# Performance work log

Hardware: AMD Instinct MI355X
Metric: run time of the kernel (lower is better)

The kernel has to match this reference:

```python
import jax, jax.numpy as jnp
import numpy as np

N_NODES = 100000
N_EDGES = 1000000
IN_DIM, HID_DIM, OUT_DIM = 256, 128, 128


def setup_inputs() -> dict:
    key = jax.random.key(0)
    ks = jax.random.split(key, 6)
    return {
        "x1": jax.random.normal(ks[0], (N_NODES, IN_DIM), jnp.float32),
        "edge_index1": jax.random.randint(ks[1], (2, N_EDGES), 0, N_NODES, jnp.int64),
        "x2": jax.random.normal(ks[2], (N_NODES, IN_DIM), jnp.float32),
        "edge_index2": jax.random.randint(ks[3], (2, N_EDGES), 0, N_NODES, jnp.int64),
        "W0": jax.random.normal(ks[4], (IN_DIM, HID_DIM), jnp.float32) * (1.0 / np.sqrt(IN_DIM)),
        "b0": jnp.zeros((HID_DIM,), jnp.float32),
        "W1": jax.random.normal(ks[5], (HID_DIM, OUT_DIM), jnp.float32) * (1.0 / np.sqrt(HID_DIM)),
        "b1": jnp.zeros((OUT_DIM,), jnp.float32),
        "p1": 0,
        "p2": 0,
    }


def _gcn_backbone(x, edge_index, W0, b0, W1, b1):
    # PyG GCNConv: add self-loops, symmetric norm D^-1/2 (A+I) D^-1/2,
    # h = x @ W, aggregate src->dst, add bias.
    n = x.shape[0]
    loops = jnp.arange(n, dtype=edge_index.dtype)
    src = jnp.concatenate([edge_index[0], loops])
    dst = jnp.concatenate([edge_index[1], loops])
    deg = jax.ops.segment_sum(jnp.ones_like(dst, jnp.float32), dst, num_segments=n)
    dinv = jnp.where(deg > 0, jax.lax.rsqrt(deg), 0.0)
    coef = (dinv[src] * dinv[dst])[:, None]  # [E+n, 1]

    def conv(h, W, b):
        h = h @ W  # [n, d_out]
        return jax.ops.segment_sum(h[src] * coef, dst, num_segments=n) + b

    h = jax.nn.relu(conv(x, W0, b0))
    # dropout with p=0 / eval mode is identity
    return conv(h, W1, b1)


def _colnorm(h):
    # (h - mean(0)) / std(0), torch std is unbiased (ddof=1)
    mu = h.mean(axis=0)
    sd = h.std(axis=0, ddof=1)
    return (h - mu) / sd


def reference(x1, edge_index1, x2, edge_index2, W0, b0, W1, b1, p1, p2):
    h1 = _gcn_backbone(x1, edge_index1, W0, b0, W1, b1)
    h2 = _gcn_backbone(x2, edge_index2, W0, b0, W1, b1)
    return _colnorm(h1), _colnorm(h2)
```

## Files before the change

### kernel.cpp

```cpp
#include <hip/hip_runtime.h>

#define CDIV(a,b) (((a)+(b)-1)/(b))

typedef __bf16 bf16x8 __attribute__((ext_vector_type(8)));
typedef float  f32x4  __attribute__((ext_vector_type(4)));

__device__ __forceinline__ ushort f2bf(float f) {
    uint u = __float_as_uint(f);
    uint r = u + 0x7fffu + ((u >> 16) & 1u);
    return (ushort)(r >> 16);
}
__device__ __forceinline__ float bf_lo(uint p) { return __uint_as_float(p << 16); }
__device__ __forceinline__ float bf_hi(uint p) { return __uint_as_float(p & 0xffff0000u); }


__global__ __launch_bounds__(256) void binA_k(const int* __restrict__ src,
                                              const int* __restrict__ dst, int E,
                                              int NB, int CAP,
                                              int* __restrict__ bcur,
                                              uint* __restrict__ binned) {
    __shared__ uint hist[512];
    __shared__ uint cur[512];
    const int t = threadIdx.x;
    for (int i = t; i < NB; i += 256) hist[i] = 0;
    __syncthreads();

    const int e0 = blockIdx.x * 4096;
    const int e1 = min(e0 + 4096, E);
    for (int e = e0 + t; e < e1; e += 256)
        atomicAdd(&hist[dst[e] >> 8], 1u);
    __syncthreads();

    for (int i = t; i < NB; i += 256) {
        uint c = hist[i];
        cur[i] = c ? (uint)atomicAdd(&bcur[i], (int)c) : 0u;
    }
    __syncthreads();

    for (int e = e0 + t; e < e1; e += 256) {
        int d = dst[e];
        int b = d >> 8;
        uint p = atomicAdd(&cur[b], 1u);
        if (p < (uint)CAP)
            binned[(size_t)b * CAP + p] = ((uint)src[e] << 8) | (uint)(d & 255);
    }
}

__global__ __launch_bounds__(256) void binB_k(const uint* __restrict__ binned,
                                              const int* __restrict__ bcur,
                                              int N, int CAP,
                                              int* __restrict__ csr,
                                              int* __restrict__ start,
                                              int* __restrict__ degc,
                                              float* __restrict__ dinv) {
    __shared__ uint hist[256];
    __shared__ uint cur[256];
    __shared__ uint wsum[4];
    const int b = blockIdx.x;
    const int t = threadIdx.x;
    int cnt = bcur[b];
    if (cnt > CAP) cnt = CAP;
    const uint* be = binned + (size_t)b * CAP;

    hist[t] = 0;
    __syncthreads();
    for (int e = t; e < cnt; e += 256) atomicAdd(&hist[be[e] & 255u], 1u);
    __syncthreads();

    uint v = hist[t];
    uint inc = v;
#pragma unroll
    for (int off = 1; off < 64; off <<= 1) {
        uint n = __shfl_up(inc, off);
        if ((t & 63) >= off) inc += n;
    }
    if ((t & 63) == 63) wsum[t >> 6] = inc;
    __syncthreads();
    uint wo = 0;
    if ((t >> 6) >= 1) wo += wsum[0];
    if ((t >> 6) >= 2) wo += wsum[1];
    if ((t >> 6) >= 3) wo += wsum[2];
    uint excl = wo + inc - v;
    cur[t] = excl;
    __syncthreads();

    const int base = b * CAP;
    for (int e = t; e < cnt; e += 256) {
        uint w = be[e];
        uint p = atomicAdd(&cur[w & 255u], 1u);
        csr[base + (int)p] = (int)(w >> 8);
    }

    int node = b * 256 + t;
    if (node < N) {
        start[node] = base + (int)excl;
        degc[node]  = (int)v;
        dinv[node]  = rsqrtf((float)(v + 1));
    }
}


__global__ __launch_bounds__(256) void pack_w_k(const float* __restrict__ W,
                                                ushort* __restrict__ Wp, int K) {
    int idx = blockIdx.x * 256 + threadIdx.x;
    int total = (K / 32) * 8 * 64;
    if (idx >= total) return;
    int l  = idx & 63;
    int nf = (idx >> 6) & 7;
    int kb = idx >> 9;
    int col = nf * 16 + (l & 15);
    int k0  = kb * 32 + (l >> 4) * 8;
    ushort o[8];
#pragma unroll
    for (int j = 0; j < 8; ++j) o[j] = f2bf(W[(size_t)(k0 + j) * 128 + col]);
    *reinterpret_cast<float4*>(Wp + (size_t)idx * 8) = *reinterpret_cast<float4*>(o);
}


template <int K, typename TIn>
__global__ __launch_bounds__(256) void gemm_mfma(const TIn* __restrict__ X,
                                                 const float4* __restrict__ Wp,
                                                 const float* __restrict__ dinv,
                                                 ushort* __restrict__ C, int N) {
    constexpr int SLOTS = K / 8;
    __shared__ ushort As[128 * K];

    const int t    = threadIdx.x;
    const int lane = t & 63;
    const int w    = t >> 6;
    const int row0 = blockIdx.x * 128;

    for (int i = t; i < 128 * SLOTS; i += 256) {
        int r = i / SLOTS;
        int c = i % SLOTS;
        int grow = row0 + r;
        ushort av[8];
        if (grow < N) {
            if constexpr (sizeof(TIn) == 4) {
                const float* px = (const float*)X + (size_t)grow * K + c * 8;
                float4 v0 = *reinterpret_cast<const float4*>(px);
                float4 v1 = *reinterpret_cast<const float4*>(px + 4);
                av[0] = f2bf(v0.x); av[1] = f2bf(v0.y); av[2] = f2bf(v0.z); av[3] = f2bf(v0.w);
                av[4] = f2bf(v1.x); av[5] = f2bf(v1.y); av[6] = f2bf(v1.z); av[7] = f2bf(v1.w);
            } else {
                const ushort* px = (const ushort*)X + (size_t)grow * K + c * 8;
                *reinterpret_cast<float4*>(av) = *reinterpret_cast<const float4*>(px);
            }
        } else {
#pragma unroll
            for (int j = 0; j < 8; ++j) av[j] = 0;
        }
        int cs = c ^ (r & 7);
        *reinterpret_cast<float4*>(&As[r * K + cs * 8]) = *reinterpret_cast<float4*>(av);
    }
    __syncthreads();

    f32x4 acc[2][8] = {};

#pragma unroll
    for (int kb = 0; kb < K / 32; ++kb) {
        bf16x8 bfr[8];
#pragma unroll
        for (int nf = 0; nf < 8; ++nf)
            bfr[nf] = *reinterpret_cast<const bf16x8*>(Wp + (size_t)(kb * 8 + nf) * 64 + lane);
#pragma unroll
        for (int mf = 0; mf < 2; ++mf) {
            int r = w * 32 + mf * 16 + (lane & 15);
            int c = kb * 4 + (lane >> 4);
            int cs = c ^ (r & 7);
            bf16x8 a = *reinterpret_cast<const bf16x8*>(&As[r * K + cs * 8]);
#pragma unroll
            for (int nf = 0; nf < 8; ++nf)
                acc[mf][nf] = __builtin_amdgcn_mfma_f32_16x16x32_bf16(a, bfr[nf], acc[mf][nf], 0, 0, 0);
        }
    }

#pragma unroll
    for (int mf = 0; mf < 2; ++mf) {
        const int rb = row0 + w * 32 + mf * 16 + ((lane >> 4) << 2);
#pragma unroll
        for (int i = 0; i < 4; ++i) {
            int row = rb + i;
            if (row < N) {
                float dr = dinv[row];
#pragma unroll
                for (int nf = 0; nf < 8; ++nf)
                    C[(size_t)row * 128 + nf * 16 + (lane & 15)] = f2bf(acc[mf][nf][i] * dr);
            }
        }
    }
}


template <int RELU, typename TOut>
__global__ __launch_bounds__(256) void agg_k(const ushort* __restrict__ Hin,
                                             TOut* __restrict__ Hout,
                                             const int* __restrict__ csr,
                                             const int* __restrict__ start,
                                             const int* __restrict__ degc,
                                             const float* __restrict__ dinv,
                                             const float* __restrict__ bias,
                                             int N) {
    const int wid  = threadIdx.x >> 6;
    const int lane = threadIdx.x & 63;
    const int v = blockIdx.x * 4 + wid;
    if (v >= N) return;

    float dv = dinv[v];
    int s   = start[v];
    int end = s + degc[v];

    const uint* base = reinterpret_cast<const uint*>(Hin);
    uint hp = base[(size_t)v * 64 + lane];
    float ax = bf_lo(hp);
    float ay = bf_hi(hp);

    for (int bs = s; bs < end; bs += 64) {
        int m = end - bs;
        if (m > 64) m = 64;
        int u_l = 0;
        if (lane < m) u_l = csr[bs + lane];
        int e = 0;
        for (; e + 8 <= m; e += 8) {
            uint p[8];
#pragma unroll
            for (int j = 0; j < 8; ++j) {
                int u = __shfl(u_l, e + j);
                p[j] = base[(size_t)u * 64 + lane];
            }
#pragma unroll
            for (int j = 0; j < 8; ++j) { ax += bf_lo(p[j]); ay += bf_hi(p[j]); }
        }
        if (e + 4 <= m) {
            uint p[4];
#pragma unroll
            for (int j = 0; j < 4; ++j) {
                int u = __shfl(u_l, e + j);
                p[j] = base[(size_t)u * 64 + lane];
            }
#pragma unroll
            for (int j = 0; j < 4; ++j) { ax += bf_lo(p[j]); ay += bf_hi(p[j]); }
            e += 4;
        }
        for (; e < m; ++e) {
            int u = __shfl(u_l, e);
            uint p = base[(size_t)u * 64 + lane];
            ax += bf_lo(p);
            ay += bf_hi(p);
        }
    }

    float2 b = reinterpret_cast<const float2*>(bias)[lane];
    float ox = fmaf(dv, ax, b.x);
    float oy = fmaf(dv, ay, b.y);
    if (RELU) {
        ox = fmaxf(ox, 0.f);
        oy = fmaxf(oy, 0.f);
    }
    if constexpr (sizeof(TOut) == 2) {
        uint packed = (uint)f2bf(ox) | ((uint)f2bf(oy) << 16);
        reinterpret_cast<uint*>(Hout)[(size_t)v * 64 + lane] = packed;
    } else {
        reinterpret_cast<float2*>(Hout)[(size_t)v * 64 + lane] = make_float2(ox, oy);
    }
}


__global__ __launch_bounds__(256) void colstats_k(const ushort* __restrict__ H,
                                                  float* __restrict__ stats, int N) {
    __shared__ float4 red[4][64];
    const int t  = threadIdx.x;
    const int cp = t & 63;
    const int rg = t >> 6;
    const int r0 = blockIdx.x * 512;
    const int r1 = min(r0 + 512, N);

    const uint* base = reinterpret_cast<const uint*>(H);
    float sx = 0.f, qx = 0.f, sy = 0.f, qy = 0.f;
    for (int r = r0 + rg; r < r1; r += 4) {
        uint p = base[(size_t)r * 64 + cp];
        float a = bf_lo(p), b = bf_hi(p);
        sx += a; qx = fmaf(a, a, qx);
        sy += b; qy = fmaf(b, b, qy);
    }
    red[rg][cp] = make_float4(sx, qx, sy, qy);
    __syncthreads();
    if (rg == 0) {
        float4 a0 = red[0][cp], a1 = red[1][cp], a2 = red[2][cp], a3 = red[3][cp];
        float* st = stats + (size_t)(blockIdx.x & 7) * 256;
        atomicAdd(&st[cp * 2],           a0.x + a1.x + a2.x + a3.x);
        atomicAdd(&st[cp * 2 + 1],       a0.z + a1.z + a2.z + a3.z);
        atomicAdd(&st[128 + cp * 2],     a0.y + a1.y + a2.y + a3.y);
        atomicAdd(&st[128 + cp * 2 + 1], a0.w + a1.w + a2.w + a3.w);
    }
}


__global__ __launch_bounds__(256) void colnorm_k(const ushort* __restrict__ H,
                                                 const float* __restrict__ stats,
                                                 float* __restrict__ Out, int N) {
    __shared__ float mu_s[128], rs_s[128];
    const int t = threadIdx.x;
    if (t < 128) {
        float s = 0.f, q = 0.f;
#pragma unroll
        for (int sl = 0; sl < 8; ++sl) {
            s += stats[sl * 256 + t];
            q += stats[sl * 256 + 128 + t];
        }
        float mu = s / (float)N;
        float var = (q - s * mu) / (float)(N - 1);
        mu_s[t] = mu;
        rs_s[t] = rsqrtf(var);
    }
    __syncthreads();

    size_t total = (size_t)N * 16;
    size_t stride = (size_t)gridDim.x * 256;
    for (size_t i = (size_t)blockIdx.x * 256 + t; i < total; i += stride) {
        uint4 p = reinterpret_cast<const uint4*>(H)[i];
        int c0 = ((int)(i & 15)) * 8;
        float o[8] = {bf_lo(p.x), bf_hi(p.x), bf_lo(p.y), bf_hi(p.y),
                      bf_lo(p.z), bf_hi(p.z), bf_lo(p.w), bf_hi(p.w)};
        float4 r0, r1;
        r0.x = (o[0] - mu_s[c0 + 0]) * rs_s[c0 + 0];
        r0.y = (o[1] - mu_s[c0 + 1]) * rs_s[c0 + 1];
        r0.z = (o[2] - mu_s[c0 + 2]) * rs_s[c0 + 2];
        r0.w = (o[3] - mu_s[c0 + 3]) * rs_s[c0 + 3];
        r1.x = (o[4] - mu_s[c0 + 4]) * rs_s[c0 + 4];
        r1.y = (o[5] - mu_s[c0 + 5]) * rs_s[c0 + 5];
        r1.z = (o[6] - mu_s[c0 + 6]) * rs_s[c0 + 6];
        r1.w = (o[7] - mu_s[c0 + 7]) * rs_s[c0 + 7];
        reinterpret_cast<float4*>(Out)[i * 2]     = r0;
        reinterpret_cast<float4*>(Out)[i * 2 + 1] = r1;
    }
}


extern "C" void kernel_launch(void* const* d_in, const int* in_sizes, int n_in,
                              void* d_out, int out_size, void* d_ws, size_t ws_size,
                              hipStream_t stream) {
    const float* x1  = (const float*)d_in[0];
    const int*   ei1 = (const int*)d_in[1];
    const float* x2  = (const float*)d_in[2];
    const int*   ei2 = (const int*)d_in[3];
    const float* W0  = (const float*)d_in[4];
    const float* b0  = (const float*)d_in[5];
    const float* W1  = (const float*)d_in[6];
    const float* b1  = (const float*)d_in[7];

    const int N  = in_sizes[0] / 256;
    const int E1 = in_sizes[1] / 2;
    const int E2 = in_sizes[3] / 2;
    const int Emax = E1 > E2 ? E1 : E2;

    const int NB  = CDIV(N, 256);
    int cap = (Emax / NB) * 8 / 5 + 1024;
    const int CAP = (cap + 1023) & ~1023;

    char* base = (char*)d_ws;
    size_t off = 0;
    auto carve = [&](size_t bytes) -> char* {
        char* p = base + off;
        off = (off + bytes + 255) & ~(size_t)255;
        return p;
    };
    ushort* hA    = (ushort*)carve((size_t)N * 128 * 2);
    ushort* hB    = (ushort*)carve((size_t)N * 128 * 2);
    float*  dinv  = (float*)carve((size_t)N * 4);
    int*    degc  = (int*)carve((size_t)N * 4);
    int*    startA= (int*)carve((size_t)N * 4);
    int*    csr   = (int*)carve((size_t)NB * CAP * 4);
    ushort* Wp0   = (ushort*)carve((256 / 32) * 8 * 64 * 8 * 2);
    ushort* Wp1   = (ushort*)carve((128 / 32) * 8 * 64 * 8 * 2);
    float*  stats = (float*)carve(8 * 256 * 4);
    int*    bcur  = (int*)carve((size_t)NB * 4);
    uint*   binned = (uint*)hA;

    pack_w_k<<<CDIV((256 / 32) * 8 * 64, 256), 256, 0, stream>>>(W0, Wp0, 256);
    pack_w_k<<<CDIV((128 / 32) * 8 * 64, 256), 256, 0, stream>>>(W1, Wp1, 128);

    for (int g = 0; g < 2; ++g) {
        const float* x  = g ? x2 : x1;
        const int*   ei = g ? ei2 : ei1;
        const int    E  = g ? E2 : E1;
        float* outg = (float*)d_out + (size_t)g * N * 128;

        hipMemsetAsync(bcur, 0, (size_t)NB * 4, stream);
        hipMemsetAsync(stats, 0, 8 * 256 * 4, stream);

        binA_k<<<CDIV(E, 4096), 256, 0, stream>>>(ei, ei + E, E, NB, CAP, bcur, binned);
        binB_k<<<NB, 256, 0, stream>>>(binned, bcur, N, CAP, csr, startA, degc, dinv);

        gemm_mfma<256, float><<<CDIV(N, 128), 256, 0, stream>>>(
            x, (const float4*)Wp0, dinv, hA, N);
        agg_k<1, ushort><<<CDIV(N, 4), 256, 0, stream>>>(
            hA, hB, csr, startA, degc, dinv, b0, N);

        gemm_mfma<128, ushort><<<CDIV(N, 128), 256, 0, stream>>>(
            hB, (const float4*)Wp1, dinv, hA, N);
        agg_k<0, ushort><<<CDIV(N, 4), 256, 0, stream>>>(
            hA, hB, csr, startA, degc, dinv, b1, N);

        colstats_k<<<CDIV(N, 512), 256, 0, stream>>>(hB, stats, N);
        colnorm_k<<<1024, 256, 0, stream>>>(hB, stats, outg, N);
    }
}
```

Baseline: 505.8 us.

## Load GEMM A tiles via direct global-to-LDS copies with 64-row blocks

Result: no change. 499.4 us (-1.3%).

```diff
diff --git a/kernel.cpp b/kernel.cpp
--- a/kernel.cpp
+++ b/kernel.cpp
@@ -12,6 +12,12 @@
 }
 __device__ __forceinline__ float bf_lo(uint p) { return __uint_as_float(p << 16); }
 __device__ __forceinline__ float bf_hi(uint p) { return __uint_as_float(p & 0xffff0000u); }
+
+__device__ __forceinline__ void glds16(const void* g, void* l) {
+    __builtin_amdgcn_global_load_lds(
+        (const __attribute__((address_space(1))) void*)g,
+        (__attribute__((address_space(3))) void*)l, 16, 0, 0);
+}
 
 
 __global__ __launch_bounds__(256) void binA_k(const int* __restrict__ src,
@@ -122,40 +128,37 @@
                                                  const float4* __restrict__ Wp,
                                                  const float* __restrict__ dinv,
                                                  ushort* __restrict__ C, int N) {
-    constexpr int SLOTS = K / 8;
-    __shared__ ushort As[128 * K];
+    constexpr int ROWB = K * (int)sizeof(TIn);
+    __shared__ char As[64 * ROWB];
 
     const int t    = threadIdx.x;
     const int lane = t & 63;
     const int w    = t >> 6;
-    const int row0 = blockIdx.x * 128;
-
-    for (int i = t; i < 128 * SLOTS; i += 256) {
-        int r = i / SLOTS;
-        int c = i % SLOTS;
-        int grow = row0 + r;
-        ushort av[8];
-        if (grow < N) {
-            if constexpr (sizeof(TIn) == 4) {
-                const float* px = (const float*)X + (size_t)grow * K + c * 8;
-                float4 v0 = *reinterpret_cast<const float4*>(px);
-                float4 v1 = *reinterpret_cast<const float4*>(px + 4);
-                av[0] = f2bf(v0.x); av[1] = f2bf(v0.y); av[2] = f2bf(v0.z); av[3] = f2bf(v0.w);
-                av[4] = f2bf(v1.x); av[5] = f2bf(v1.y); av[6] = f2bf(v1.z); av[7] = f2bf(v1.w);
-            } else {
-                const ushort* px = (const ushort*)X + (size_t)grow * K + c * 8;
-                *reinterpret_cast<float4*>(av) = *reinterpret_cast<const float4*>(px);
-            }
-        } else {
-#pragma unroll
-            for (int j = 0; j < 8; ++j) av[j] = 0;
-        }
-        int cs = c ^ (r & 7);
-        *reinterpret_cast<float4*>(&As[r * K + cs * 8]) = *reinterpret_cast<float4*>(av);
-    }
-    __syncthreads();
-
-    f32x4 acc[2][8] = {};
+    const int row0 = blockIdx.x * 64;
+
+    if constexpr (sizeof(TIn) == 4) {
+#pragma unroll
+        for (int i = 0; i < 16; ++i) {
+            int rr   = w * 16 + i;
+            int grow = min(row0 + rr, N - 1);
+            const float* src = (const float*)X + (size_t)grow * K + (size_t)(lane ^ (i & 7)) * 4;
+            glds16(src, As + (size_t)rr * ROWB);
+        }
+    } else {
+#pragma unroll
+        for (int i = 0; i < 4; ++i) {
+            int rr   = w * 16 + i * 4 + (lane >> 4);
+            int grow = min(row0 + rr, N - 1);
+            int slot = (lane & 15) ^ (rr & 7);
+            const ushort* src = (const ushort*)X + (size_t)grow * K + (size_t)slot * 8;
+            glds16(src, As + (size_t)(w * 16 + i * 4) * ROWB);
+        }
+    }
+    __syncthreads();
+
+    f32x4 acc[8] = {};
+    const int r  = w * 16 + (lane & 15);
+    const int kc = lane >> 4;
 
 #pragma unroll
     for (int kb = 0; kb < K / 32; ++kb) {
@@ -163,30 +166,34 @@
 #pragma unroll
         for (int nf = 0; nf < 8; ++nf)
             bfr[nf] = *reinterpret_cast<const bf16x8*>(Wp + (size_t)(kb * 8 + nf) * 64 + lane);
-#pragma unroll
-        for (int mf = 0; mf < 2; ++mf) {
-            int r = w * 32 + mf * 16 + (lane & 15);
-            int c = kb * 4 + (lane >> 4);
-            int cs = c ^ (r & 7);
-            bf16x8 a = *reinterpret_cast<const bf16x8*>(&As[r * K + cs * 8]);
+
+        bf16x8 a;
+        if constexpr (sizeof(TIn) == 4) {
+            int s0 = (kb * 8 + kc * 2) ^ (r & 7);
+            int s1 = (kb * 8 + kc * 2 + 1) ^ (r & 7);
+            f32x4 a0 = *reinterpret_cast<const f32x4*>(&As[(size_t)r * ROWB + (size_t)s0 * 16]);
+            f32x4 a1 = *reinterpret_cast<const f32x4*>(&As[(size_t)r * ROWB + (size_t)s1 * 16]);
+            a[0] = (__bf16)a0[0]; a[1] = (__bf16)a0[1]; a[2] = (__bf16)a0[2]; a[3] = (__bf16)a0[3];
+            a[4] = (__bf16)a1[0]; a[5] = (__bf16)a1[1]; a[6] = (__bf16)a1[2]; a[7] = (__bf16)a1[3];
+        } else {
+            int s = (kb * 4 + kc) ^ (r & 7);
+            a = *reinterpret_cast<const bf16x8*>(&As[(size_t)r * ROWB + (size_t)s * 16]);
+        }
+
+#pragma unroll
+        for (int nf = 0; nf < 8; ++nf)
+            acc[nf] = __builtin_amdgcn_mfma_f32_16x16x32_bf16(a, bfr[nf], acc[nf], 0, 0, 0);
+    }
+
+    const int rb = row0 + w * 16 + ((lane >> 4) << 2);
+#pragma unroll
+    for (int i = 0; i < 4; ++i) {
+        int row = rb + i;
+        if (row < N) {
+            float dr = dinv[row];
 #pragma unroll
             for (int nf = 0; nf < 8; ++nf)
-                acc[mf][nf] = __builtin_amdgcn_mfma_f32_16x16x32_bf16(a, bfr[nf], acc[mf][nf], 0, 0, 0);
-        }
-    }
-
-#pragma unroll
-    for (int mf = 0; mf < 2; ++mf) {
-        const int rb = row0 + w * 32 + mf * 16 + ((lane >> 4) << 2);
-#pragma unroll
-        for (int i = 0; i < 4; ++i) {
-            int row = rb + i;
-            if (row < N) {
-                float dr = dinv[row];
-#pragma unroll
-                for (int nf = 0; nf < 8; ++nf)
-                    C[(size_t)row * 128 + nf * 16 + (lane & 15)] = f2bf(acc[mf][nf][i] * dr);
-            }
+                C[(size_t)row * 128 + nf * 16 + (lane & 15)] = f2bf(acc[nf][i] * dr);
         }
     }
 }
@@ -392,12 +399,12 @@
         binA_k<<<CDIV(E, 4096), 256, 0, stream>>>(ei, ei + E, E, NB, CAP, bcur, binned);
         binB_k<<<NB, 256, 0, stream>>>(binned, bcur, N, CAP, csr, startA, degc, dinv);
 
-        gemm_mfma<256, float><<<CDIV(N, 128), 256, 0, stream>>>(
+        gemm_mfma<256, float><<<CDIV(N, 64), 256, 0, stream>>>(
             x, (const float4*)Wp0, dinv, hA, N);
         agg_k<1, ushort><<<CDIV(N, 4), 256, 0, stream>>>(
             hA, hB, csr, startA, degc, dinv, b0, N);
 
-        gemm_mfma<128, ushort><<<CDIV(N, 128), 256, 0, stream>>>(
+        gemm_mfma<128, ushort><<<CDIV(N, 64), 256, 0, stream>>>(
             hB, (const float4*)Wp1, dinv, hA, N);
         agg_k<0, ushort><<<CDIV(N, 4), 256, 0, stream>>>(
             hA, hB, csr, startA, degc, dinv, b1, N);
```
